# Performance work log

Measured on AMD Instinct MI355X. Metric: run time of the kernel, lower is better.

Reference implementation:

```python
import jax, jax.numpy as jnp
import numpy as np

N_NODES = 100000
N_FEAT = 128
HID = 8
HEADS1 = 8
OUT2 = 32
NEG_SLOPE = 0.2


def gat_conv(x, W, a_src, a_dst, b, src, dst, n_nodes, concat):
    # x: [N, Fin], W: [Fin, H*C], a_src/a_dst: [H, C], b: [H*C] or [C]
    H, C = a_src.shape
    h = (x @ W).reshape(n_nodes, H, C)                      # [N, H, C]
    e_src = jnp.sum(h * a_src, axis=-1)                     # [N, H]
    e_dst = jnp.sum(h * a_dst, axis=-1)                     # [N, H]
    e = jax.nn.leaky_relu(e_src[src] + e_dst[dst], NEG_SLOPE)  # [E, H]
    m = jax.ops.segment_max(e, dst, num_segments=n_nodes)   # [N, H] (self-loops => no empty segment)
    ex = jnp.exp(e - m[dst])                                # [E, H]
    denom = jax.ops.segment_sum(ex, dst, num_segments=n_nodes)
    alpha = ex / denom[dst]                                 # [E, H]
    out = jax.ops.segment_sum(alpha[:, :, None] * h[src], dst, num_segments=n_nodes)  # [N, H, C]
    out = out.reshape(n_nodes, H * C) if concat else out.mean(axis=1)
    return out + b


def setup_inputs() -> dict:
    key = jax.random.key(0)
    ks = jax.random.split(key, 12)
    x = jax.random.normal(ks[0], (N_NODES, N_FEAT), dtype=jnp.float32)
    edge_index = jax.random.randint(ks[1], (2, 3200000), 0, N_NODES, dtype=jnp.int64)
    s1 = 1.0 / np.sqrt(N_FEAT)
    s2 = 1.0 / np.sqrt(HID * HEADS1)
    return {
        "x": x,
        "edge_index": edge_index,
        "W1": jax.random.normal(ks[2], (N_FEAT, HEADS1 * HID), dtype=jnp.float32) * s1,
        "a_src1": jax.random.normal(ks[3], (HEADS1, HID), dtype=jnp.float32) * s2,
        "a_dst1": jax.random.normal(ks[4], (HEADS1, HID), dtype=jnp.float32) * s2,
        "b1": jnp.zeros((HEADS1 * HID,), dtype=jnp.float32),
        "W2": jax.random.normal(ks[5], (HEADS1 * HID, OUT2), dtype=jnp.float32) * s2,
        "a_src2": jax.random.normal(ks[6], (1, OUT2), dtype=jnp.float32) * (1.0 / np.sqrt(OUT2)),
        "a_dst2": jax.random.normal(ks[7], (1, OUT2), dtype=jnp.float32) * (1.0 / np.sqrt(OUT2)),
        "b2": jnp.zeros((OUT2,), dtype=jnp.float32),
        "Wr": jax.random.normal(ks[8], (OUT2, 1), dtype=jnp.float32) * (1.0 / np.sqrt(OUT2)),
        "br": jnp.zeros((1,), dtype=jnp.float32),
    }


def reference(x, edge_index, W1, a_src1, a_dst1, b1, W2, a_src2, a_dst2, b2, Wr, br):
    n = x.shape[0]
    # PyG GATConv default add_self_loops=True
    loops = jnp.arange(n, dtype=edge_index.dtype)
    src = jnp.concatenate([edge_index[0], loops])
    dst = jnp.concatenate([edge_index[1], loops])
    h = gat_conv(x, W1, a_src1, a_dst1, b1, src, dst, n, concat=True)   # [N, 64]
    h = jax.nn.elu(h)
    h = gat_conv(h, W2, a_src2, a_dst2, b2, src, dst, n, concat=False)  # [N, 32]
    pooled = jnp.sum(h, axis=0, keepdims=True)                          # SumAggregation -> [1, 32]
    return pooled @ Wr + br                                             # [1, 1]
```

## Files before the change

### kernel.cpp

```cpp
#include <hip/hip_runtime.h>
#include <math.h>

#define NEG_SLOPE 0.2f
#define FIN 128
#define H1 8
#define F1 64
#define F2 32

#define SHIFT 5
#define BW 32
#define CAPL 2048
#define CAP_G 1408
#define NBMAX 4096

#define SB_SHIFT 11
#define NSBMAX 64
#define P_CHUNK 2048
#define BPS 35
#define SBCAP (BPS * P_CHUNK)

typedef unsigned short ushort_t;
typedef unsigned int uint_t;

#define LO16(u) __uint_as_float((u) << 16)
#define HI16(u) __uint_as_float((u) & 0xffff0000u)

#define FOLDQ(x) { x += __shfl_xor(x, 8, 64); x += __shfl_xor(x, 16, 64); x += __shfl_xor(x, 32, 64); }
#define FOLD64(x) { x += __shfl_xor(x, 1, 64); x += __shfl_xor(x, 2, 64); x += __shfl_xor(x, 4, 64); \
                    x += __shfl_xor(x, 8, 64); x += __shfl_xor(x, 16, 64); x += __shfl_xor(x, 32, 64); }

static __device__ __forceinline__ ushort_t f2bf(float f) {
    uint_t u = __float_as_uint(f);
    u = (u + 0x7FFFu + ((u >> 16) & 1u)) >> 16;
    return (ushort_t)u;
}
static __device__ __forceinline__ uint_t packAB(float e) {
    return (uint_t)f2bf(__expf(e)) | ((uint_t)f2bf(__expf(NEG_SLOPE * e)) << 16);
}

__global__ void gemm1_kernel(const float* __restrict__ x, const float* __restrict__ W1,
                             const float* __restrict__ a_src, const float* __restrict__ a_dst,
                             ushort_t* __restrict__ h1, uint_t* __restrict__ sp,
                             float* __restrict__ ed, int N) {
    __shared__ float xs[16][FIN];
    int tid = threadIdx.x;
    int n0 = blockIdx.x * 16;
    for (int i = tid; i < 16 * FIN; i += 256) {
        int nn = n0 + (i >> 7);
        xs[i >> 7][i & 127] = (nn < N) ? x[(size_t)nn * FIN + (i & 127)] : 0.f;
    }
    __syncthreads();
    int wv = tid >> 6, j = tid & 63;
    int nb = wv << 2;
    float a0 = 0.f, a1 = 0.f, a2 = 0.f, a3 = 0.f;
#pragma unroll 2
    for (int k = 0; k < FIN; k += 4) {
        float w0 = W1[(k + 0) * F1 + j];
        float w1 = W1[(k + 1) * F1 + j];
        float w2 = W1[(k + 2) * F1 + j];
        float w3 = W1[(k + 3) * F1 + j];
        float4 x0 = *(const float4*)&xs[nb + 0][k];
        float4 x1 = *(const float4*)&xs[nb + 1][k];
        float4 x2 = *(const float4*)&xs[nb + 2][k];
        float4 x3 = *(const float4*)&xs[nb + 3][k];
        a0 = fmaf(x0.x, w0, fmaf(x0.y, w1, fmaf(x0.z, w2, fmaf(x0.w, w3, a0))));
        a1 = fmaf(x1.x, w0, fmaf(x1.y, w1, fmaf(x1.z, w2, fmaf(x1.w, w3, a1))));
        a2 = fmaf(x2.x, w0, fmaf(x2.y, w1, fmaf(x2.z, w2, fmaf(x2.w, w3, a2))));
        a3 = fmaf(x3.x, w0, fmaf(x3.y, w1, fmaf(x3.z, w2, fmaf(x3.w, w3, a3))));
    }
    float as = a_src[j], ad = a_dst[j];
    float av[4] = {a0, a1, a2, a3};
#pragma unroll
    for (int t = 0; t < 4; ++t) {
        int n = n0 + nb + t;
        if (n >= N) break;
        h1[(size_t)n * F1 + j] = f2bf(av[t]);
        float vs = av[t] * as;
        float vd = av[t] * ad;
#pragma unroll
        for (int off = 4; off >= 1; off >>= 1) {
            vs += __shfl_down(vs, off, 8);
            vd += __shfl_down(vd, off, 8);
        }
        if ((j & 7) == 0) {
            sp[n * H1 + (j >> 3)] = packAB(vs);
            ed[n * H1 + (j >> 3)] = vd;
        }
    }
}

__global__ void zerob_kernel(int* __restrict__ bcnt, int* __restrict__ boff,
                             int NB, float* __restrict__ pooled, int capg,
                             int* __restrict__ sbcnt, int nsb,
                             uint_t* __restrict__ sp1, ushort_t* __restrict__ h1,
                             int* __restrict__ ctrs, int N) {
    int t = blockIdx.x * blockDim.x + threadIdx.x;
    int stride = gridDim.x * blockDim.x;
    for (int i = t; i < NB; i += stride) {
        bcnt[i] = 0;
        if (capg) boff[i] = i * capg;
    }
    for (int i = t; i < nsb; i += stride) sbcnt[i] = 0;
    if (t < H1) sp1[(size_t)N * H1 + t] = 0u;
    if (t >= 8 && t < 8 + F1) h1[(size_t)N * F1 + (t - 8)] = 0;
    if (t == 72) pooled[0] = 0.f;
    if (t == 73) ctrs[0] = 0;
    if (t == 74) ctrs[1] = 0;
}

__global__ void __launch_bounds__(256, 4)
part1_kernel(const int* __restrict__ ei, int E, int N,
             int* __restrict__ sbcnt, uint_t* __restrict__ sbdata) {
    __shared__ int hist[NSBMAX];
    __shared__ int loff[NSBMAX];
    __shared__ int lcur[NSBMAX];
    __shared__ int gb[NSBMAX];
    __shared__ uint_t buf[P_CHUNK];
    __shared__ unsigned char sbarr[P_CHUNK];
    int tid = threadIdx.x;
    int NSB = (N + ((1 << SB_SHIFT) - 1)) >> SB_SHIFT;
    for (int i = tid; i < NSB; i += 256) hist[i] = 0;
    __syncthreads();
    int EN = E + N;
    int base = blockIdx.x * P_CHUNK;
    int m = EN - base; if (m > P_CHUNK) m = P_CHUNK;
    int t0 = base + tid * 8;
    int s[8], d[8];
    bool fast = (t0 + 8 <= E) && ((E & 3) == 0);
    if (fast) {
        int4 a = *(const int4*)&ei[t0];
        int4 b = *(const int4*)&ei[t0 + 4];
        s[0]=a.x; s[1]=a.y; s[2]=a.z; s[3]=a.w; s[4]=b.x; s[5]=b.y; s[6]=b.z; s[7]=b.w;
        int4 c = *(const int4*)&ei[E + t0];
        int4 e2 = *(const int4*)&ei[E + t0 + 4];
        d[0]=c.x; d[1]=c.y; d[2]=c.z; d[3]=c.w; d[4]=e2.x; d[5]=e2.y; d[6]=e2.z; d[7]=e2.w;
    } else {
#pragma unroll
        for (int r = 0; r < 8; ++r) {
            int t = t0 + r;
            if (t < EN) {
                if (t < E) { s[r] = ei[t]; d[r] = ei[E + t]; }
                else       { s[r] = d[r] = t - E; }
            } else d[r] = -1;
        }
    }
#pragma unroll
    for (int r = 0; r < 8; ++r)
        if (d[r] >= 0) atomicAdd(&hist[d[r] >> SB_SHIFT], 1);
    __syncthreads();
    if (tid < 64) {
        int v = (tid < NSB) ? hist[tid] : 0;
        int e = v;
#pragma unroll
        for (int o = 1; o < 64; o <<= 1) {
            int u = __shfl_up(e, o, 64);
            if (tid >= o) e += u;
        }
        e -= v;
        if (tid < NSB) {
            loff[tid] = e;
            lcur[tid] = e;
            gb[tid] = v ? atomicAdd(&sbcnt[tid], v) : 0;
        }
    }
    __syncthreads();
#pragma unroll
    for (int r = 0; r < 8; ++r)
        if (d[r] >= 0) {
            int sb = d[r] >> SB_SHIFT;
            int pos = atomicAdd(&lcur[sb], 1);
            buf[pos] = ((uint_t)s[r] << SB_SHIFT) | (uint_t)(d[r] & ((1 << SB_SHIFT) - 1));
            sbarr[pos] = (unsigned char)sb;
        }
    __syncthreads();
    for (int i = tid; i < m; i += 256) {
        int sb = sbarr[i];
        int idx = gb[sb] + (i - loff[sb]);
        if (idx < SBCAP)
            sbdata[(size_t)sb * SBCAP + idx] = buf[i];
    }
}

__global__ void __launch_bounds__(256, 4)
part2_kernel(const uint_t* __restrict__ sbdata, const int* __restrict__ sbcnt,
             int* __restrict__ bcnt, const int* __restrict__ boff,
             uint_t* __restrict__ pk) {
    __shared__ int hist[64];
    __shared__ int loff[64];
    __shared__ int lcur[64];
    __shared__ int gb[64];
    __shared__ uint_t buf[P_CHUNK];
    int tid = threadIdx.x;
    int sb = blockIdx.x / BPS;
    int base = (blockIdx.x % BPS) * P_CHUNK;
    int cnt = sbcnt[sb];
    if (cnt > SBCAP) cnt = SBCAP;
    if (base >= cnt) return;
    int m = cnt - base; if (m > P_CHUNK) m = P_CHUNK;
    if (tid < 64) hist[tid] = 0;
    __syncthreads();
    const uint_t* src = sbdata + (size_t)sb * SBCAP + base;
    uint_t v[8];
#pragma unroll
    for (int r = 0; r < 8; ++r) {
        int i = tid + r * 256;
        if (i < m) {
            v[r] = src[i];
            atomicAdd(&hist[(v[r] >> 5) & 63], 1);
        }
    }
    __syncthreads();
    if (tid < 64) {
        int c = hist[tid];
        int e = c;
#pragma unroll
        for (int o = 1; o < 64; o <<= 1) {
            int u = __shfl_up(e, o, 64);
            if (tid >= o) e += u;
        }
        e -= c;
        loff[tid] = e;
        lcur[tid] = e;
        int bucket = (sb << 6) + tid;
        gb[tid] = c ? (boff[bucket] + atomicAdd(&bcnt[bucket], c)) : 0;
    }
    __syncthreads();
#pragma unroll
    for (int r = 0; r < 8; ++r) {
        int i = tid + r * 256;
        if (i < m) {
            int lb = (v[r] >> 5) & 63;
            int pos = atomicAdd(&lcur[lb], 1);
            buf[pos] = v[r];
        }
    }
    __syncthreads();
    for (int i = tid; i < m; i += 256) {
        uint_t u = buf[i];
        int lb = (u >> 5) & 63;
        int idx = gb[lb] + (i - loff[lb]);
        pk[idx] = ((u >> SB_SHIFT) << SHIFT) | (u & (BW - 1));
    }
}

__global__ void bhist_kernel(const int* __restrict__ ei, int E, int N,
                             int* __restrict__ bcnt, int NB) {
    __shared__ int h[NBMAX];
    int tid = threadIdx.x;
    for (int i = tid; i < NB; i += 256) h[i] = 0;
    __syncthreads();
    int EN = E + N;
    int chunk = (EN + gridDim.x - 1) / gridDim.x;
    int e0 = blockIdx.x * chunk;
    int e1 = e0 + chunk; if (e1 > EN) e1 = EN;
    for (int t = e0 + tid; t < e1; t += 256) {
        int d = (t < E) ? ei[E + t] : (t - E);
        atomicAdd(&h[d >> SHIFT], 1);
    }
    __syncthreads();
    for (int i = tid; i < NB; i += 256)
        if (h[i]) atomicAdd(&bcnt[i], h[i]);
}

__global__ void bscan_kernel(const int* __restrict__ bcnt, int NB,
                             int* __restrict__ boff, int* __restrict__ bcur) {
    int lane = threadIdx.x;
    int chunk = (NB + 63) >> 6;
    int lo = lane * chunk;
    int hi = lo + chunk; if (hi > NB) hi = NB;
    int sum = 0;
    for (int i = lo; i < hi; ++i) sum += bcnt[i];
    int e = sum;
#pragma unroll
    for (int o = 1; o < 64; o <<= 1) {
        int v = __shfl_up(e, o, 64);
        if (lane >= o) e += v;
    }
    e -= sum;
    int run = e;
    for (int i = lo; i < hi; ++i) {
        int c = bcnt[i];
        boff[i] = run;
        bcur[i] = run;
        run += c;
    }
}

__global__ void bscat_kernel(const int* __restrict__ ei, int E, int N,
                             int* __restrict__ bcur, uint_t* __restrict__ pk, int NB) {
    __shared__ int lh[NBMAX];
    __shared__ int lc[NBMAX];
    int tid = threadIdx.x;
    for (int i = tid; i < NB; i += 256) lh[i] = 0;
    __syncthreads();
    int EN = E + N;
    int chunk = (EN + gridDim.x - 1) / gridDim.x;
    int e0 = blockIdx.x * chunk;
    int e1 = e0 + chunk; if (e1 > EN) e1 = EN;
    for (int t = e0 + tid; t < e1; t += 256) {
        int d = (t < E) ? ei[E + t] : (t - E);
        atomicAdd(&lh[d >> SHIFT], 1);
    }
    __syncthreads();
    for (int i = tid; i < NB; i += 256) {
        int c = lh[i];
        lc[i] = c ? atomicAdd(&bcur[i], c) : 0;
    }
    __syncthreads();
    for (int t = e0 + tid; t < e1; t += 256) {
        int s, d;
        if (t < E) { s = ei[t]; d = ei[E + t]; } else { s = d = t - E; }
        int pos = atomicAdd(&lc[d >> SHIFT], 1);
        pk[pos] = ((uint_t)s << SHIFT) | (uint_t)(d & (BW - 1));
    }
}

__global__ void __launch_bounds__(256, 8)
edge1_gather(const int* __restrict__ bcnt, const int* __restrict__ boff,
             const uint_t* __restrict__ pk,
             const uint_t* __restrict__ sp, const float* __restrict__ ed,
             const ushort_t* __restrict__ h1, float* __restrict__ o1,
             int* __restrict__ ctr, int NB, int N) {
    int tid = threadIdx.x;
    int wv = tid >> 6;
    int L = tid & 63;
    int q = L >> 3;
    int head = L & 7;
    int c8 = head << 3;
    __shared__ int ldeg[BW], loff[BW], ldgp[BW], lcur[BW];
    __shared__ int lsrc[CAPL];
    __shared__ int sbk, stot;
    for (;;) {
        if (tid == 0) sbk = atomicAdd(ctr, 1);
        __syncthreads();
        int b = sbk;
        if (b >= NB) break;
        int d0 = b << SHIFT;
        int cnt = bcnt[b];
        int gbase = boff[b];
        if (cnt <= CAPL - 8 * BW - 16) {
            if (tid < BW) ldeg[tid] = 0;
            __syncthreads();
            for (int k = tid; k < cnt; k += 256) atomicAdd(&ldeg[pk[gbase + k] & (BW - 1)], 1);
            __syncthreads();
            if (tid < BW) {
                int v = ldeg[tid];
                int vp = (v + 7) & ~7;
                int e = vp;
#pragma unroll
                for (int o = 1; o < BW; o <<= 1) {
                    int u = __shfl_up(e, o, 64);
                    if (tid >= o) e += u;
                }
                e -= vp;
                loff[tid] = e;
                lcur[tid] = e;
                ldgp[tid] = vp;
                if (tid == BW - 1) stot = e + vp;
            }
            __syncthreads();
            int tot = stot;
            for (int k = tid; k < tot + 16; k += 256) lsrc[k] = N;
            __syncthreads();
            for (int k = tid; k < cnt; k += 256) {
                uint_t v = pk[gbase + k];
                int pos = atomicAdd(&lcur[v & (BW - 1)], 1);
                lsrc[pos] = (int)(v >> SHIFT);
            }
            __syncthreads();
            for (int ld = wv * 8; ld < wv * 8 + 8; ++ld) {
                int d = d0 + ld;
                if (d >= N) break;
                int st = loff[ld], en = st + ldgp[ld];
                float edv = ed[d * H1 + head];
                float Ad = __expf(edv), Bd = __expf(NEG_SLOPE * edv);
                float a0=0.f,a1=0.f,a2=0.f,a3=0.f,a4=0.f,a5=0.f,a6=0.f,a7=0.f,ws=0.f;
                int sA = lsrc[st + q];
                uint_t UA = sp[sA * H1 + head];
                uint4 VA = *(const uint4*)(h1 + ((size_t)sA << 6) + c8);
                int sB = lsrc[st + 8 + q];
                uint_t UB = sp[sB * H1 + head];
                uint4 VB = *(const uint4*)(h1 + ((size_t)sB << 6) + c8);
                for (int k = st; k < en; k += 8) {
                    int sC = lsrc[k + 16 + q];
                    uint_t UC = sp[sC * H1 + head];
                    uint4 VC = *(const uint4*)(h1 + ((size_t)sC << 6) + c8);
                    float w = fmaxf(LO16(UA) * Ad, HI16(UA) * Bd);
                    a0 = fmaf(w, LO16(VA.x), a0); a1 = fmaf(w, HI16(VA.x), a1);
                    a2 = fmaf(w, LO16(VA.y), a2); a3 = fmaf(w, HI16(VA.y), a3);
                    a4 = fmaf(w, LO16(VA.z), a4); a5 = fmaf(w, HI16(VA.z), a5);
                    a6 = fmaf(w, LO16(VA.w), a6); a7 = fmaf(w, HI16(VA.w), a7);
                    ws += w;
                    UA = UB; VA = VB;
                    UB = UC; VB = VC;
                }
                FOLDQ(a0); FOLDQ(a1); FOLDQ(a2); FOLDQ(a3);
                FOLDQ(a4); FOLDQ(a5); FOLDQ(a6); FOLDQ(a7); FOLDQ(ws);
                if (q == 0) {
                    float inv = 1.f / ws;
                    float4 r0; r0.x = a0*inv; r0.y = a1*inv; r0.z = a2*inv; r0.w = a3*inv;
                    float4 r1; r1.x = a4*inv; r1.y = a5*inv; r1.z = a6*inv; r1.w = a7*inv;
                    float* dp = o1 + (size_t)d * F1 + c8;
                    *(float4*)dp = r0;
                    *(float4*)(dp + 4) = r1;
                }
            }
        } else {
            for (int ld = wv * 8; ld < wv * 8 + 8; ++ld) {
                int d = d0 + ld;
                if (d >= N) break;
                float edv = ed[d * H1 + head];
                float Ad = __expf(edv), Bd = __expf(NEG_SLOPE * edv);
                float a0=0.f,a1=0.f,a2=0.f,a3=0.f,a4=0.f,a5=0.f,a6=0.f,a7=0.f,ws=0.f;
                for (int k0 = 0; k0 < cnt; k0 += 8) {
                    int idx = k0 + q;
                    bool ok = idx < cnt;
                    uint_t v = pk[gbase + (ok ? idx : 0)];
                    int s = (int)(v >> SHIFT);
                    bool mm = ok && ((int)(v & (BW - 1)) == ld);
                    uint_t U = sp[s * H1 + head];
                    uint4 V = *(const uint4*)(h1 + ((size_t)s << 6) + c8);
                    float w = mm ? fmaxf(LO16(U) * Ad, HI16(U) * Bd) : 0.f;
                    a0 = fmaf(w, LO16(V.x), a0); a1 = fmaf(w, HI16(V.x), a1);
                    a2 = fmaf(w, LO16(V.y), a2); a3 = fmaf(w, HI16(V.y), a3);
                    a4 = fmaf(w, LO16(V.z), a4); a5 = fmaf(w, HI16(V.z), a5);
                    a6 = fmaf(w, LO16(V.w), a6); a7 = fmaf(w, HI16(V.w), a7);
                    ws += w;
                }
                FOLDQ(a0); FOLDQ(a1); FOLDQ(a2); FOLDQ(a3);
                FOLDQ(a4); FOLDQ(a5); FOLDQ(a6); FOLDQ(a7); FOLDQ(ws);
                if (q == 0) {
                    float inv = 1.f / ws;
                    float4 r0; r0.x = a0*inv; r0.y = a1*inv; r0.z = a2*inv; r0.w = a3*inv;
                    float4 r1; r1.x = a4*inv; r1.y = a5*inv; r1.z = a6*inv; r1.w = a7*inv;
                    float* dp = o1 + (size_t)d * F1 + c8;
                    *(float4*)dp = r0;
                    *(float4*)(dp + 4) = r1;
                }
            }
        }
    }
}

__global__ void gemm2_kernel(const float* __restrict__ o1, const float* __restrict__ b1,
                             const float* __restrict__ W2,
                             const float* __restrict__ a_src2, const float* __restrict__ a_dst2,
                             const float* __restrict__ Wr,
                             uint2* __restrict__ rec, float* __restrict__ ed2, int N) {
    if (blockIdx.x == 0 && threadIdx.x == 0) {
        uint2 z; z.x = 0u; z.y = 0u;
        rec[N] = z;
    }
    int half = threadIdx.x >> 5;
    int n = blockIdx.x * 8 + half;
    int j = threadIdx.x & 31;
    __shared__ float a1s[8][F1];
    if (n < N) {
#pragma unroll
        for (int r = 0; r < 2; ++r) {
            int k = r * 32 + j;
            float v = o1[(size_t)n * F1 + k] + b1[k];
            a1s[half][k] = v > 0.f ? v : expm1f(v);
        }
    }
    __syncthreads();
    if (n >= N) return;
    float acc = 0.f;
#pragma unroll
    for (int k = 0; k < F1; ++k) acc = fmaf(a1s[half][k], W2[k * F2 + j], acc);
    float vs = acc * a_src2[j];
    float vd = acc * a_dst2[j];
    float vg = acc * Wr[j];
#pragma unroll
    for (int off = 16; off >= 1; off >>= 1) {
        vs += __shfl_down(vs, off, 32);
        vd += __shfl_down(vd, off, 32);
        vg += __shfl_down(vg, off, 32);
    }
    if (j == 0) {
        uint2 r; r.x = packAB(vs); r.y = __float_as_uint(vg);
        rec[n] = r;
        ed2[n] = vd;
    }
}

__global__ void __launch_bounds__(256, 8)
edge2_gather(const int* __restrict__ bcnt, const int* __restrict__ boff,
             const uint_t* __restrict__ pk,
             const uint2* __restrict__ rec, const float* __restrict__ ed2,
             const float* __restrict__ b2, const float* __restrict__ Wr,
             float* __restrict__ pooled, int* __restrict__ ctr, int NB, int N) {
    int tid = threadIdx.x;
    int wv = tid >> 6;
    int L = tid & 63;
    __shared__ int ldeg[BW], loff[BW], ldgp[BW], lcur[BW];
    __shared__ int lsrc[CAPL];
    __shared__ int sbk, stot;
    __shared__ float ls[4];
    float t0 = (L < F2) ? b2[L] * Wr[L] : 0.f;
    FOLD64(t0);
    float b2w = t0;
    float part = 0.f;
    for (;;) {
        if (tid == 0) sbk = atomicAdd(ctr, 1);
        __syncthreads();
        int b = sbk;
        if (b >= NB) break;
        int d0 = b << SHIFT;
        int cnt = bcnt[b];
        int gbase = boff[b];
        if (cnt <= CAPL - 8 * BW - 16) {
            if (tid < BW) ldeg[tid] = 0;
            __syncthreads();
            for (int k = tid; k < cnt; k += 256) atomicAdd(&ldeg[pk[gbase + k] & (BW - 1)], 1);
            __syncthreads();
            if (tid < BW) {
                int v = ldeg[tid];
                int vp = (v + 7) & ~7;
                int e = vp;
#pragma unroll
                for (int o = 1; o < BW; o <<= 1) {
                    int u = __shfl_up(e, o, 64);
                    if (tid >= o) e += u;
                }
                e -= vp;
                loff[tid] = e;
                lcur[tid] = e;
                ldgp[tid] = vp;
                if (tid == BW - 1) stot = e + vp;
            }
            __syncthreads();
            int tot = stot;
            for (int k = tid; k < tot + 16; k += 256) lsrc[k] = N;
            __syncthreads();
            for (int k = tid; k < cnt; k += 256) {
                uint_t v = pk[gbase + k];
                int pos = atomicAdd(&lcur[v & (BW - 1)], 1);
                lsrc[pos] = (int)(v >> SHIFT);
            }
            __syncthreads();
            for (int ld = wv * 8; ld < wv * 8 + 8; ++ld) {
                int d = d0 + ld;
                if (d >= N) break;
                int st = loff[ld], en = st + ldgp[ld];
                float edv = ed2[d];
                float Ad = __expf(edv), Bd = __expf(NEG_SLOPE * edv);
                float acc = 0.f, wsm = 0.f;
                for (int k = st; k < en; k += 64) {
                    int i = k + L;
                    bool ok = i < en;
                    int s = lsrc[ok ? i : st];
                    uint2 r = rec[s];
                    float w = ok ? fmaxf(LO16(r.x) * Ad, HI16(r.x) * Bd) : 0.f;
                    acc = fmaf(w, __uint_as_float(r.y), acc);
                    wsm += w;
                }
                FOLD64(acc); FOLD64(wsm);
                part += acc / wsm + b2w;
            }
        } else {
            for (int ld = wv * 8; ld < wv * 8 + 8; ++ld) {
                int d = d0 + ld;
                if (d >= N) break;
                float edv = ed2[d];
                float Ad = __expf(edv), Bd = __expf(NEG_SLOPE * edv);
                float acc = 0.f, wsm = 0.f;
                for (int k0 = 0; k0 < cnt; k0 += 64) {
                    int i = k0 + L;
                    bool ok = i < cnt;
                    uint_t v = pk[gbase + (ok ? i : 0)];
                    int s = (int)(v >> SHIFT);
                    bool mm = ok && ((int)(v & (BW - 1)) == ld);
                    uint2 r = rec[s];
                    float w = mm ? fmaxf(LO16(r.x) * Ad, HI16(r.x) * Bd) : 0.f;
                    acc = fmaf(w, __uint_as_float(r.y), acc);
                    wsm += w;
                }
                FOLD64(acc); FOLD64(wsm);
                part += acc / wsm + b2w;
            }
        }
    }
    if (L == 0) ls[wv] = part;
    __syncthreads();
    if (tid == 0) atomicAdd(pooled, ls[0] + ls[1] + ls[2] + ls[3]);
}

__global__ void final_kernel(const float* __restrict__ pooled, const float* __restrict__ br,
                             float* __restrict__ out) {
    if (threadIdx.x == 0 && blockIdx.x == 0) out[0] = pooled[0] + br[0];
}

static inline size_t al128(size_t v) { return (v + 127) & ~(size_t)127; }

extern "C" void kernel_launch(void* const* d_in, const int* in_sizes, int n_in,
                              void* d_out, int out_size, void* d_ws, size_t ws_size,
                              hipStream_t stream) {
    const float* x    = (const float*)d_in[0];
    const int*   ei   = (const int*)d_in[1];
    const float* W1   = (const float*)d_in[2];
    const float* a_s1 = (const float*)d_in[3];
    const float* a_d1 = (const float*)d_in[4];
    const float* b1   = (const float*)d_in[5];
    const float* W2   = (const float*)d_in[6];
    const float* a_s2 = (const float*)d_in[7];
    const float* a_d2 = (const float*)d_in[8];
    const float* b2   = (const float*)d_in[9];
    const float* Wr   = (const float*)d_in[10];
    const float* br   = (const float*)d_in[11];
    float* out = (float*)d_out;

    int N = in_sizes[0] / FIN;
    int E = in_sizes[1] / 2;
    size_t n = (size_t)N;
    int NB = (N + BW - 1) >> SHIFT;
    int NSB = (N + ((1 << SB_SHIFT) - 1)) >> SB_SHIFT;

    char* ws = (char*)d_ws;
    size_t off_o1  = 0;
    size_t off_sp1 = al128(off_o1 + n * 256);
    size_t off_ed1 = al128(off_sp1 + n * 32 + 32);
    size_t off_h1  = al128(off_ed1 + n * 32);
    size_t off_pk  = al128(off_h1 + n * 128 + 128);
    float*    o1   = (float*)(ws + off_o1);
    uint_t*   sp1  = (uint_t*)(ws + off_sp1);
    float*    ed1  = (float*)(ws + off_ed1);
    ushort_t* h1   = (ushort_t*)(ws + off_h1);
    uint_t*   pk   = (uint_t*)(ws + off_pk);
    size_t pk_static = (size_t)NB * CAP_G * 4;
    size_t pk_exact  = (size_t)(E + N) * 4;
    uint_t* sbdata = (uint_t*)ws;
    bool use_static = (NSB <= NSBMAX) &&
                      ((size_t)NSB * SBCAP * 4 <= n * 256) &&
                      (ws_size >= off_pk + pk_static + (size_t)NBMAX * 16 +
                                  (size_t)NSBMAX * 4 + 128);
    char* tail = ws + off_pk + (use_static ? pk_static : pk_exact);
    int*      bcnt  = (int*)tail;
    int*      boff  = (int*)(tail + NBMAX * 4);
    int*      bcur  = (int*)(tail + NBMAX * 8);
    int*      sbcnt = (int*)(tail + NBMAX * 12);
    float*  pooled  = (float*)(tail + NBMAX * 12 + NSBMAX * 4);
    int*      ctrs  = (int*)(tail + NBMAX * 12 + NSBMAX * 4 + 8);
    uint2* rec = (uint2*)h1;
    float* ed2 = ed1;

    int egrid = NB < 2048 ? NB : 2048;

    zerob_kernel<<<8, 256, 0, stream>>>(bcnt, boff, NB, pooled,
                                        use_static ? CAP_G : 0, sbcnt, NSB,
                                        sp1, h1, ctrs, N);
    if (use_static) {
        int EN = E + N;
        int G1 = (EN + P_CHUNK - 1) / P_CHUNK;
        part1_kernel<<<G1, 256, 0, stream>>>(ei, E, N, sbcnt, sbdata);
        part2_kernel<<<NSB * BPS, 256, 0, stream>>>(sbdata, sbcnt, bcnt, boff, pk);
        gemm1_kernel<<<(N + 15) / 16, 256, 0, stream>>>(x, W1, a_s1, a_d1, h1, sp1, ed1, N);
    } else {
        gemm1_kernel<<<(N + 15) / 16, 256, 0, stream>>>(x, W1, a_s1, a_d1, h1, sp1, ed1, N);
        bhist_kernel<<<256, 256, 0, stream>>>(ei, E, N, bcnt, NB);
        bscan_kernel<<<1, 64, 0, stream>>>(bcnt, NB, boff, bcur);
        bscat_kernel<<<256, 256, 0, stream>>>(ei, E, N, bcur, pk, NB);
    }
    edge1_gather<<<egrid, 256, 0, stream>>>(bcnt, boff, pk, sp1, ed1, h1, o1,
                                            ctrs + 0, NB, N);
    gemm2_kernel<<<(N + 7) / 8, 256, 0, stream>>>(o1, b1, W2, a_s2, a_d2, Wr, rec, ed2, N);
    edge2_gather<<<egrid, 256, 0, stream>>>(bcnt, boff, pk, rec, ed2, b2, Wr, pooled,
                                            ctrs + 1, NB, N);
    final_kernel<<<1, 64, 0, stream>>>(pooled, br, out);
}
```

Before: 458.7 us.

## Remap edge1 gather lanes to 4 channels each and drop padded source lists

The layer-1 gather kernel now gives each lane 4 feature channels (8-byte loads), so 16 lanes cover a destination row and 4 edges are processed in parallel, instead of 8 lanes of 8 channels each. Each thread handles two edges per iteration with a prefetched next pair, and the reduction needs two shuffle steps instead of three. Per-destination source lists are no longer padded to a multiple of 8 with sentinel entries; out-of-range slots are masked by predication, which removes the fill pass and allows larger buckets on the shared-memory path. This trades wider per-lane loads for more lane-level parallelism across edges, at the cost of extra bounds checks and redundant attention-weight loads per head.

```diff
diff --git a/kernel.cpp b/kernel.cpp
--- a/kernel.cpp
+++ b/kernel.cpp
@@ -25,7 +25,7 @@
 #define LO16(u) __uint_as_float((u) << 16)
 #define HI16(u) __uint_as_float((u) & 0xffff0000u)
 
-#define FOLDQ(x) { x += __shfl_xor(x, 8, 64); x += __shfl_xor(x, 16, 64); x += __shfl_xor(x, 32, 64); }
+#define FOLDQ4(x) { x += __shfl_xor(x, 16, 64); x += __shfl_xor(x, 32, 64); }
 #define FOLD64(x) { x += __shfl_xor(x, 1, 64); x += __shfl_xor(x, 2, 64); x += __shfl_xor(x, 4, 64); \
                     x += __shfl_xor(x, 8, 64); x += __shfl_xor(x, 16, 64); x += __shfl_xor(x, 32, 64); }
 
@@ -324,12 +324,12 @@
     int tid = threadIdx.x;
     int wv = tid >> 6;
     int L = tid & 63;
-    int q = L >> 3;
-    int head = L & 7;
-    int c8 = head << 3;
-    __shared__ int ldeg[BW], loff[BW], ldgp[BW], lcur[BW];
+    int q = L >> 4;
+    int c4 = (L & 15) << 2;
+    int hL = (L & 15) >> 1;
+    __shared__ int ldeg[BW], loff[BW], lcur[BW];
     __shared__ int lsrc[CAPL];
-    __shared__ int sbk, stot;
+    __shared__ int sbk;
     for (;;) {
         if (tid == 0) sbk = atomicAdd(ctr, 1);
         __syncthreads();
@@ -338,29 +338,23 @@
         int d0 = b << SHIFT;
         int cnt = bcnt[b];
         int gbase = boff[b];
-        if (cnt <= CAPL - 8 * BW - 16) {
+        if (cnt <= CAPL) {
             if (tid < BW) ldeg[tid] = 0;
             __syncthreads();
             for (int k = tid; k < cnt; k += 256) atomicAdd(&ldeg[pk[gbase + k] & (BW - 1)], 1);
             __syncthreads();
             if (tid < BW) {
                 int v = ldeg[tid];
-                int vp = (v + 7) & ~7;
-                int e = vp;
+                int e = v;
 #pragma unroll
                 for (int o = 1; o < BW; o <<= 1) {
                     int u = __shfl_up(e, o, 64);
                     if (tid >= o) e += u;
                 }
-                e -= vp;
+                e -= v;
                 loff[tid] = e;
                 lcur[tid] = e;
-                ldgp[tid] = vp;
-                if (tid == BW - 1) stot = e + vp;
-            }
-            __syncthreads();
-            int tot = stot;
-            for (int k = tid; k < tot + 16; k += 256) lsrc[k] = N;
+            }
             __syncthreads();
             for (int k = tid; k < cnt; k += 256) {
                 uint_t v = pk[gbase + k];
@@ -371,71 +365,84 @@
             for (int ld = wv * 8; ld < wv * 8 + 8; ++ld) {
                 int d = d0 + ld;
                 if (d >= N) break;
-                int st = loff[ld], en = st + ldgp[ld];
-                float edv = ed[d * H1 + head];
+                int st = loff[ld], en = st + ldeg[ld];
+                float edv = ed[d * H1 + hL];
                 float Ad = __expf(edv), Bd = __expf(NEG_SLOPE * edv);
-                float a0=0.f,a1=0.f,a2=0.f,a3=0.f,a4=0.f,a5=0.f,a6=0.f,a7=0.f,ws=0.f;
-                int sA = lsrc[st + q];
-                uint_t UA = sp[sA * H1 + head];
-                uint4 VA = *(const uint4*)(h1 + ((size_t)sA << 6) + c8);
-                int sB = lsrc[st + 8 + q];
-                uint_t UB = sp[sB * H1 + head];
-                uint4 VB = *(const uint4*)(h1 + ((size_t)sB << 6) + c8);
+                float ax = 0.f, ay = 0.f, az = 0.f, aw = 0.f, wsum = 0.f;
+                uint_t U0, U1; uint2 V0, V1;
+                {
+                    int i0 = st + q, i1 = st + 4 + q;
+                    bool ok0 = i0 < en, ok1 = i1 < en;
+                    int s0 = lsrc[ok0 ? i0 : st];
+                    int s1 = lsrc[ok1 ? i1 : st];
+                    uint_t u0 = sp[s0 * H1 + hL];
+                    uint_t u1 = sp[s1 * H1 + hL];
+                    V0 = *(const uint2*)(h1 + ((size_t)s0 << 6) + c4);
+                    V1 = *(const uint2*)(h1 + ((size_t)s1 << 6) + c4);
+                    U0 = ok0 ? u0 : 0u;
+                    U1 = ok1 ? u1 : 0u;
+                }
                 for (int k = st; k < en; k += 8) {
-                    int sC = lsrc[k + 16 + q];
-                    uint_t UC = sp[sC * H1 + head];
-                    uint4 VC = *(const uint4*)(h1 + ((size_t)sC << 6) + c8);
-                    float w = fmaxf(LO16(UA) * Ad, HI16(UA) * Bd);
-                    a0 = fmaf(w, LO16(VA.x), a0); a1 = fmaf(w, HI16(VA.x), a1);
-                    a2 = fmaf(w, LO16(VA.y), a2); a3 = fmaf(w, HI16(VA.y), a3);
-                    a4 = fmaf(w, LO16(VA.z), a4); a5 = fmaf(w, HI16(VA.z), a5);
-                    a6 = fmaf(w, LO16(VA.w), a6); a7 = fmaf(w, HI16(VA.w), a7);
-                    ws += w;
-                    UA = UB; VA = VB;
-                    UB = UC; VB = VC;
-                }
-                FOLDQ(a0); FOLDQ(a1); FOLDQ(a2); FOLDQ(a3);
-                FOLDQ(a4); FOLDQ(a5); FOLDQ(a6); FOLDQ(a7); FOLDQ(ws);
+                    uint_t N0, N1; uint2 P0, P1;
+                    {
+                        int i0 = k + 8 + q, i1 = k + 12 + q;
+                        bool ok0 = i0 < en, ok1 = i1 < en;
+                        int s0 = lsrc[ok0 ? i0 : st];
+                        int s1 = lsrc[ok1 ? i1 : st];
+                        uint_t u0 = sp[s0 * H1 + hL];
+                        uint_t u1 = sp[s1 * H1 + hL];
+                        P0 = *(const uint2*)(h1 + ((size_t)s0 << 6) + c4);
+                        P1 = *(const uint2*)(h1 + ((size_t)s1 << 6) + c4);
+                        N0 = ok0 ? u0 : 0u;
+                        N1 = ok1 ? u1 : 0u;
+                    }
+                    float w0 = fmaxf(LO16(U0) * Ad, HI16(U0) * Bd);
+                    float w1 = fmaxf(LO16(U1) * Ad, HI16(U1) * Bd);
+                    ax = fmaf(w0, LO16(V0.x), ax);
+                    ay = fmaf(w0, HI16(V0.x), ay);
+                    az = fmaf(w0, LO16(V0.y), az);
+                    aw = fmaf(w0, HI16(V0.y), aw);
+                    ax = fmaf(w1, LO16(V1.x), ax);
+                    ay = fmaf(w1, HI16(V1.x), ay);
+                    az = fmaf(w1, LO16(V1.y), az);
+                    aw = fmaf(w1, HI16(V1.y), aw);
+                    wsum += w0 + w1;
+                    U0 = N0; U1 = N1; V0 = P0; V1 = P1;
+                }
+                FOLDQ4(ax); FOLDQ4(ay); FOLDQ4(az); FOLDQ4(aw); FOLDQ4(wsum);
                 if (q == 0) {
-                    float inv = 1.f / ws;
-                    float4 r0; r0.x = a0*inv; r0.y = a1*inv; r0.z = a2*inv; r0.w = a3*inv;
-                    float4 r1; r1.x = a4*inv; r1.y = a5*inv; r1.z = a6*inv; r1.w = a7*inv;
-                    float* dp = o1 + (size_t)d * F1 + c8;
-                    *(float4*)dp = r0;
-                    *(float4*)(dp + 4) = r1;
+                    float inv = 1.f / wsum;
+                    float4 r; r.x = ax * inv; r.y = ay * inv; r.z = az * inv; r.w = aw * inv;
+                    *(float4*)(o1 + (size_t)d * F1 + c4) = r;
                 }
             }
         } else {
             for (int ld = wv * 8; ld < wv * 8 + 8; ++ld) {
                 int d = d0 + ld;
                 if (d >= N) break;
-                float edv = ed[d * H1 + head];
+                float edv = ed[d * H1 + hL];
                 float Ad = __expf(edv), Bd = __expf(NEG_SLOPE * edv);
-                float a0=0.f,a1=0.f,a2=0.f,a3=0.f,a4=0.f,a5=0.f,a6=0.f,a7=0.f,ws=0.f;
-                for (int k0 = 0; k0 < cnt; k0 += 8) {
+                float ax = 0.f, ay = 0.f, az = 0.f, aw = 0.f, wsum = 0.f;
+                for (int k0 = 0; k0 < cnt; k0 += 4) {
                     int idx = k0 + q;
                     bool ok = idx < cnt;
                     uint_t v = pk[gbase + (ok ? idx : 0)];
                     int s = (int)(v >> SHIFT);
-                    bool mm = ok && ((int)(v & (BW - 1)) == ld);
-                    uint_t U = sp[s * H1 + head];
-                    uint4 V = *(const uint4*)(h1 + ((size_t)s << 6) + c8);
-                    float w = mm ? fmaxf(LO16(U) * Ad, HI16(U) * Bd) : 0.f;
-                    a0 = fmaf(w, LO16(V.x), a0); a1 = fmaf(w, HI16(V.x), a1);
-                    a2 = fmaf(w, LO16(V.y), a2); a3 = fmaf(w, HI16(V.y), a3);
-                    a4 = fmaf(w, LO16(V.z), a4); a5 = fmaf(w, HI16(V.z), a5);
-                    a6 = fmaf(w, LO16(V.w), a6); a7 = fmaf(w, HI16(V.w), a7);
-                    ws += w;
-                }
-                FOLDQ(a0); FOLDQ(a1); FOLDQ(a2); FOLDQ(a3);
-                FOLDQ(a4); FOLDQ(a5); FOLDQ(a6); FOLDQ(a7); FOLDQ(ws);
+                    bool m = ok && ((int)(v & (BW - 1)) == ld);
+                    uint_t u = sp[(uint_t)s * H1 + hL];
+                    float w = m ? fmaxf(LO16(u) * Ad, HI16(u) * Bd) : 0.f;
+                    uint2 hv = *(const uint2*)(h1 + ((size_t)s << 6) + c4);
+                    ax = fmaf(w, LO16(hv.x), ax);
+                    ay = fmaf(w, HI16(hv.x), ay);
+                    az = fmaf(w, LO16(hv.y), az);
+                    aw = fmaf(w, HI16(hv.y), aw);
+                    wsum += w;
+                }
+                FOLDQ4(ax); FOLDQ4(ay); FOLDQ4(az); FOLDQ4(aw); FOLDQ4(wsum);
                 if (q == 0) {
-                    float inv = 1.f / ws;
-                    float4 r0; r0.x = a0*inv; r0.y = a1*inv; r0.z = a2*inv; r0.w = a3*inv;
-                    float4 r1; r1.x = a4*inv; r1.y = a5*inv; r1.z = a6*inv; r1.w = a7*inv;
-                    float* dp = o1 + (size_t)d * F1 + c8;
-                    *(float4*)dp = r0;
-                    *(float4*)(dp + 4) = r1;
+                    float inv = 1.f / wsum;
+                    float4 r; r.x = ax * inv; r.y = ay * inv; r.z = az * inv; r.w = aw * inv;
+                    *(float4*)(o1 + (size_t)d * F1 + c4) = r;
                 }
             }
         }
```

Result: no change. 454.6 us (-0.9%).
